# Kernel optimization log

Hardware: AMD Instinct MI355X
Metric: run time of the kernel (lower is better)

Reference implementation:

```python
import jax, jax.numpy as jnp
import numpy as np

MIN_STATES = 4
MAX_STATES = 64
B, S, D_IN, D_ST = 32, 2048, 1024, 512


def _linear_init(k, out_dim, in_dim):
    k1, k2 = jax.random.split(k)
    s = 1.0 / np.sqrt(in_dim)
    W = jax.random.uniform(k1, (out_dim, in_dim), minval=-s, maxval=s, dtype=jnp.float32)
    b = jax.random.uniform(k2, (out_dim,), minval=-s, maxval=s, dtype=jnp.float32)
    return W, b


def setup_inputs() -> dict:
    key = jax.random.key(0)
    ks = jax.random.split(key, 8)
    # complexity estimator MLP: D_IN -> D_ST -> D_ST//2 -> 1
    W1, b1 = _linear_init(ks[0], D_ST, D_IN)
    W2, b2 = _linear_init(ks[1], D_ST // 2, D_ST)
    W3, b3 = _linear_init(ks[2], 1, D_ST // 2)
    # importance scorer MLP: D_ST -> D_ST//2 -> 1
    Ws1, bs1 = _linear_init(ks[3], D_ST // 2, D_ST)
    Ws2, bs2 = _linear_init(ks[4], 1, D_ST // 2)
    state_bank = jax.random.normal(ks[5], (MAX_STATES, D_ST), dtype=jnp.float32) * 0.02
    temperature = jnp.ones((1,), dtype=jnp.float32)
    x = jax.random.normal(ks[6], (B, S, D_IN), dtype=jnp.float32)
    return dict(x=x, W1=W1, b1=b1, W2=W2, b2=b2, W3=W3, b3=b3,
                Ws1=Ws1, bs1=bs1, Ws2=Ws2, bs2=bs2,
                state_bank=state_bank, temperature=temperature)


def reference(x, W1, b1, W2, b2, W3, b3, Ws1, bs1, Ws2, bs2, state_bank, temperature):
    # --- complexity: mean-pool over seq, 3-layer MLP with sigmoid ---
    x_pooled = x.mean(axis=1)                                   # [B, D_IN]
    h = jax.nn.relu(x_pooled @ W1.T + b1)                       # [B, D_ST]
    h = jax.nn.relu(h @ W2.T + b2)                              # [B, D_ST//2]
    complexity = jax.nn.sigmoid(h @ W3.T + b3)[:, 0]            # [B]
    # --- importance over state bank: 2-layer MLP + tempered softmax ---
    hs = jax.nn.relu(state_bank @ Ws1.T + bs1)                  # [MAX_STATES, D_ST//2]
    imp_logits = (hs @ Ws2.T + bs2)[:, 0]                       # [MAX_STATES]
    temp = jnp.maximum(jnp.abs(temperature), 0.1)[0]
    importance = jax.nn.softmax(imp_logits / temp)              # [MAX_STATES]
    # --- per-sample number of active states ---
    num_states = jnp.clip(
        jnp.round(MIN_STATES + complexity * (MAX_STATES - MIN_STATES)).astype(jnp.int32),
        MIN_STATES, MAX_STATES)                                 # [B]
    # --- vectorized top-k mask: rank of each state in descending importance ---
    order = jnp.argsort(-importance)                            # [MAX_STATES]
    ranks = jnp.argsort(order)                                  # ranks[i] = position of state i
    state_mask = ranks[None, :] < num_states[:, None]           # [B, MAX_STATES] bool
    allocated_states = jnp.broadcast_to(state_bank[None], (x.shape[0],) + state_bank.shape)
    return allocated_states, state_mask
```

## Files before the change

kernel.cpp:

```cpp
#include <hip/hip_runtime.h>

#define BB 32
#define SS 2048
#define DIN 1024
#define DST 512
#define DH 256
#define NST 64
#define SC 32
#define CHUNKS (SS / SC)

__device__ __forceinline__ float dot4(float4 a, float4 b) {
    return a.x * b.x + a.y * b.y + a.z * b.z + a.w * b.w;
}

__global__ void k1_pool_bcast(const float* __restrict__ x, const float* __restrict__ bank,
                              float* __restrict__ partial, float* __restrict__ out) {
    int blk = blockIdx.x;
    int t = threadIdx.x;
    if (blk < 2048) {
        int b = blk >> 6;
        int c = blk & 63;
        const float4* xp = (const float4*)(x + ((size_t)b * SS + (size_t)c * SC) * DIN);
        float4 acc = make_float4(0.f, 0.f, 0.f, 0.f);
#pragma unroll
        for (int s = 0; s < SC; ++s) {
            float4 v = xp[s * (DIN / 4) + t];
            acc.x += v.x; acc.y += v.y; acc.z += v.z; acc.w += v.w;
        }
        ((float4*)(partial + (size_t)blk * DIN))[t] = acc;
    } else {
        int idx = (blk - 2048) * 256 + t;
        ((float4*)out)[idx] = ((const float4*)bank)[idx & 8191];
    }
}

__global__ void k2_pool2(const float* __restrict__ partial, float* __restrict__ pooled) {
    int b = blockIdx.x;
    int t = threadIdx.x;
    const float4* src = (const float4*)(partial + (size_t)b * CHUNKS * DIN);
    float4 acc = make_float4(0.f, 0.f, 0.f, 0.f);
#pragma unroll 8
    for (int c = 0; c < CHUNKS; ++c) {
        float4 v = src[c * (DIN / 4) + t];
        acc.x += v.x; acc.y += v.y; acc.z += v.z; acc.w += v.w;
    }
    const float invS = 1.0f / (float)SS;
    acc.x *= invS; acc.y *= invS; acc.z *= invS; acc.w *= invS;
    ((float4*)(pooled + (size_t)b * DIN))[t] = acc;
}

__global__ void k3_layer1(const float* __restrict__ pooled,
                          const float* __restrict__ W1, const float* __restrict__ b1,
                          const float* __restrict__ Ws1, const float* __restrict__ bs1,
                          const float* __restrict__ bank,
                          float* __restrict__ h1, float* __restrict__ hs) {
    int g = blockIdx.x;
    int t = threadIdx.x;
    if (g < 64) {
        int b = t & 31;
        int j = g * 8 + (t >> 5);
        const float4* w = (const float4*)(W1 + (size_t)j * DIN);
        const float4* p = (const float4*)(pooled + (size_t)b * DIN);
        float a0 = 0.f, a1 = 0.f;
#pragma unroll 8
        for (int k = 0; k < DIN / 4; k += 2) {
            a0 += dot4(w[k], p[k]);
            a1 += dot4(w[k + 1], p[k + 1]);
        }
        h1[(size_t)b * DST + j] = fmaxf(a0 + a1 + b1[j], 0.f);
    } else {
        int g2 = g - 64;
        int i = t & 63;
        int j = g2 * 4 + (t >> 6);
        const float4* w = (const float4*)(Ws1 + (size_t)j * DST);
        const float4* s = (const float4*)(bank + (size_t)i * DST);
        float a0 = 0.f, a1 = 0.f;
#pragma unroll 8
        for (int k = 0; k < DST / 4; k += 2) {
            a0 += dot4(w[k], s[k]);
            a1 += dot4(w[k + 1], s[k + 1]);
        }
        hs[(size_t)i * DH + j] = fmaxf(a0 + a1 + bs1[j], 0.f);
    }
}

__global__ void k4_layer2(const float* __restrict__ h1,
                          const float* __restrict__ W2, const float* __restrict__ b2,
                          const float* __restrict__ hs,
                          const float* __restrict__ Ws2, const float* __restrict__ bs2,
                          const float* __restrict__ W3,
                          float* __restrict__ zpart, float* __restrict__ imp) {
    int g = blockIdx.x;
    int t = threadIdx.x;
    if (g < 32) {
        __shared__ float s_z[8][32];
        int b = t & 31;
        int jq = t >> 5;
        int j = g * 8 + jq;
        const float4* w = (const float4*)(W2 + (size_t)j * DST);
        const float4* p = (const float4*)(h1 + (size_t)b * DST);
        float a0 = 0.f, a1 = 0.f;
#pragma unroll 8
        for (int k = 0; k < DST / 4; k += 2) {
            a0 += dot4(w[k], p[k]);
            a1 += dot4(w[k + 1], p[k + 1]);
        }
        float h2v = fmaxf(a0 + a1 + b2[j], 0.f);
        s_z[jq][b] = h2v * W3[j];
        __syncthreads();
        if (t < 32) {
            float z = 0.f;
#pragma unroll
            for (int q = 0; q < 8; ++q) z += s_z[q][t];
            zpart[g * 32 + t] = z;
        }
    } else {
        __shared__ float s_p[4][NST];
        int i = t & 63;
        int part = t >> 6;
        const float4* hv = (const float4*)(hs + (size_t)i * DH + part * 64);
        const float4* wv = (const float4*)(Ws2 + part * 64);
        float a = 0.f;
#pragma unroll
        for (int m = 0; m < 16; ++m) a += dot4(hv[m], wv[m]);
        s_p[part][i] = a;
        __syncthreads();
        if (t < NST) imp[t] = s_p[0][t] + s_p[1][t] + s_p[2][t] + s_p[3][t] + bs2[0];
    }
}

__global__ void k5_final(const float* __restrict__ zpart, const float* __restrict__ b3,
                         const float* __restrict__ imp, float* __restrict__ mask_out) {
    __shared__ float s_imp[NST];
    __shared__ int s_rank[NST];
    __shared__ int s_num[BB];
    int t = threadIdx.x;
    if (t < NST) s_imp[t] = imp[t];
    if (t < BB) {
        float z = 0.f;
        for (int g = 0; g < 32; ++g) z += zpart[g * 32 + t];
        z += b3[0];
        float cx = 1.0f / (1.0f + expf(-z));
        int ns = (int)rintf(4.0f + cx * 60.0f);
        s_num[t] = min(max(ns, 4), 64);
    }
    __syncthreads();
    if (t < NST) {
        float mine = s_imp[t];
        int r = 0;
        for (int j = 0; j < NST; ++j) {
            float o = s_imp[j];
            if (o > mine || (o == mine && j < t)) ++r;
        }
        s_rank[t] = r;
    }
    __syncthreads();
    for (int idx = t; idx < BB * NST; idx += 256)
        mask_out[idx] = (s_rank[idx & 63] < s_num[idx >> 6]) ? 1.0f : 0.0f;
}

extern "C" void kernel_launch(void* const* d_in, const int* in_sizes, int n_in,
                              void* d_out, int out_size, void* d_ws, size_t ws_size,
                              hipStream_t stream) {
    const float* x    = (const float*)d_in[0];
    const float* W1   = (const float*)d_in[1];
    const float* b1   = (const float*)d_in[2];
    const float* W2   = (const float*)d_in[3];
    const float* b2   = (const float*)d_in[4];
    const float* W3   = (const float*)d_in[5];
    const float* b3   = (const float*)d_in[6];
    const float* Ws1  = (const float*)d_in[7];
    const float* bs1  = (const float*)d_in[8];
    const float* Ws2  = (const float*)d_in[9];
    const float* bs2  = (const float*)d_in[10];
    const float* bank = (const float*)d_in[11];

    float* out = (float*)d_out;
    float* mask_out = out + (size_t)BB * NST * DST;

    float* ws = (float*)d_ws;
    float* partial = ws;
    float* pooled  = partial + (size_t)BB * CHUNKS * DIN;
    float* h1  = pooled + BB * DIN;
    float* hs  = h1 + BB * DST;
    float* zpart = hs + NST * DH;
    float* imp = zpart + 1024;

    k1_pool_bcast<<<3072, 256, 0, stream>>>(x, bank, partial, out);
    k2_pool2<<<BB, 256, 0, stream>>>(partial, pooled);
    k3_layer1<<<128, 256, 0, stream>>>(pooled, W1, b1, Ws1, bs1, bank, h1, hs);
    k4_layer2<<<33, 256, 0, stream>>>(h1, W2, b2, hs, Ws2, bs2, W3, zpart, imp);
    k5_final<<<1, 256, 0, stream>>>(zpart, b3, imp, mask_out);
}
```

Measured before the change: 121.9 us.

## Fuse pipeline into three kernels with wave-reduced matvecs

Collapses five launches into three. The importance MLP is folded into the pooling/broadcast kernel as 64 extra blocks. The second pooling stage is fused with layer 1, and layer 2 is fused with the final mask computation. Matvecs now use one wave per output row with shuffle reductions instead of one thread per row, which removes intermediate buffers and launch gaps. In exchange, the pool-2 reduction is recomputed in each of the four blocks per batch row, and layer-2 per-block work is serialized over 64 iterations.

```diff
diff --git a/kernel.cpp b/kernel.cpp
--- a/kernel.cpp
+++ b/kernel.cpp
@@ -13,30 +13,68 @@
     return a.x * b.x + a.y * b.y + a.z * b.z + a.w * b.w;
 }
 
-__global__ void k1_pool_bcast(const float* __restrict__ x, const float* __restrict__ bank,
-                              float* __restrict__ partial, float* __restrict__ out) {
+__device__ __forceinline__ float wave_reduce(float d) {
+    d += __shfl_xor(d, 1);
+    d += __shfl_xor(d, 2);
+    d += __shfl_xor(d, 4);
+    d += __shfl_xor(d, 8);
+    d += __shfl_xor(d, 16);
+    d += __shfl_xor(d, 32);
+    return d;
+}
+
+__global__ void k1_pool_imp_bcast(const float* __restrict__ x,
+                                  const float* __restrict__ bank,
+                                  const float* __restrict__ Ws1, const float* __restrict__ bs1,
+                                  const float* __restrict__ Ws2, const float* __restrict__ bs2,
+                                  float* __restrict__ partial, float* __restrict__ imp,
+                                  float* __restrict__ out) {
     int blk = blockIdx.x;
     int t = threadIdx.x;
-    if (blk < 2048) {
-        int b = blk >> 6;
-        int c = blk & 63;
+    if (blk >= 64 && blk < 64 + 2048) {
+        int task = blk - 64;
+        int b = task >> 6;
+        int c = task & 63;
         const float4* xp = (const float4*)(x + ((size_t)b * SS + (size_t)c * SC) * DIN);
         float4 acc = make_float4(0.f, 0.f, 0.f, 0.f);
-#pragma unroll
+#pragma unroll 8
         for (int s = 0; s < SC; ++s) {
             float4 v = xp[s * (DIN / 4) + t];
             acc.x += v.x; acc.y += v.y; acc.z += v.z; acc.w += v.w;
         }
-        ((float4*)(partial + (size_t)blk * DIN))[t] = acc;
+        ((float4*)(partial + (size_t)task * DIN))[t] = acc;
+    } else if (blk < 64) {
+        int i = blk;
+        int w = t >> 6, lane = t & 63;
+        __shared__ float s_zp[4];
+        const float4* brow = (const float4*)(bank + (size_t)i * DST);
+        float4 p0 = brow[lane * 2];
+        float4 p1 = brow[lane * 2 + 1];
+        float zacc = 0.f;
+        for (int jt = 0; jt < 64; ++jt) {
+            int j = jt * 4 + w;
+            const float4* wrow = (const float4*)(Ws1 + (size_t)j * DST);
+            float d = dot4(wrow[lane * 2], p0) + dot4(wrow[lane * 2 + 1], p1);
+            d = wave_reduce(d);
+            if (lane == 0) zacc += fmaxf(d + bs1[j], 0.f) * Ws2[j];
+        }
+        if (lane == 0) s_zp[w] = zacc;
+        __syncthreads();
+        if (t == 0) imp[i] = s_zp[0] + s_zp[1] + s_zp[2] + s_zp[3] + bs2[0];
     } else {
-        int idx = (blk - 2048) * 256 + t;
+        int idx = (blk - 2112) * 256 + t;
         ((float4*)out)[idx] = ((const float4*)bank)[idx & 8191];
     }
 }
 
-__global__ void k2_pool2(const float* __restrict__ partial, float* __restrict__ pooled) {
-    int b = blockIdx.x;
+__global__ void k2_h1(const float* __restrict__ partial,
+                      const float* __restrict__ W1, const float* __restrict__ b1,
+                      float* __restrict__ h1) {
+    int blk = blockIdx.x;
     int t = threadIdx.x;
+    int b = blk >> 2, jc = blk & 3;
+    __shared__ float4 s_pool[256];
+
     const float4* src = (const float4*)(partial + (size_t)b * CHUNKS * DIN);
     float4 acc = make_float4(0.f, 0.f, 0.f, 0.f);
 #pragma unroll 8
@@ -46,103 +84,55 @@
     }
     const float invS = 1.0f / (float)SS;
     acc.x *= invS; acc.y *= invS; acc.z *= invS; acc.w *= invS;
-    ((float4*)(pooled + (size_t)b * DIN))[t] = acc;
-}
+    s_pool[t] = acc;
+    __syncthreads();
 
-__global__ void k3_layer1(const float* __restrict__ pooled,
-                          const float* __restrict__ W1, const float* __restrict__ b1,
-                          const float* __restrict__ Ws1, const float* __restrict__ bs1,
-                          const float* __restrict__ bank,
-                          float* __restrict__ h1, float* __restrict__ hs) {
-    int g = blockIdx.x;
-    int t = threadIdx.x;
-    if (g < 64) {
-        int b = t & 31;
-        int j = g * 8 + (t >> 5);
-        const float4* w = (const float4*)(W1 + (size_t)j * DIN);
-        const float4* p = (const float4*)(pooled + (size_t)b * DIN);
-        float a0 = 0.f, a1 = 0.f;
-#pragma unroll 8
-        for (int k = 0; k < DIN / 4; k += 2) {
-            a0 += dot4(w[k], p[k]);
-            a1 += dot4(w[k + 1], p[k + 1]);
-        }
-        h1[(size_t)b * DST + j] = fmaxf(a0 + a1 + b1[j], 0.f);
-    } else {
-        int g2 = g - 64;
-        int i = t & 63;
-        int j = g2 * 4 + (t >> 6);
-        const float4* w = (const float4*)(Ws1 + (size_t)j * DST);
-        const float4* s = (const float4*)(bank + (size_t)i * DST);
-        float a0 = 0.f, a1 = 0.f;
-#pragma unroll 8
-        for (int k = 0; k < DST / 4; k += 2) {
-            a0 += dot4(w[k], s[k]);
-            a1 += dot4(w[k + 1], s[k + 1]);
-        }
-        hs[(size_t)i * DH + j] = fmaxf(a0 + a1 + bs1[j], 0.f);
+    int w = t >> 6, lane = t & 63;
+    float4 p[4];
+#pragma unroll
+    for (int m = 0; m < 4; ++m) p[m] = s_pool[lane * 4 + m];
+    for (int jt = 0; jt < 32; ++jt) {
+        int j = jc * 128 + jt * 4 + w;
+        const float4* wrow = (const float4*)(W1 + (size_t)j * DIN);
+        float d = 0.f;
+#pragma unroll
+        for (int m = 0; m < 4; ++m) d += dot4(wrow[lane * 4 + m], p[m]);
+        d = wave_reduce(d);
+        if (lane == 0) h1[(size_t)b * DST + j] = fmaxf(d + b1[j], 0.f);
     }
 }
 
-__global__ void k4_layer2(const float* __restrict__ h1,
-                          const float* __restrict__ W2, const float* __restrict__ b2,
-                          const float* __restrict__ hs,
-                          const float* __restrict__ Ws2, const float* __restrict__ bs2,
-                          const float* __restrict__ W3,
-                          float* __restrict__ zpart, float* __restrict__ imp) {
-    int g = blockIdx.x;
+__global__ void k3_final(const float* __restrict__ h1,
+                         const float* __restrict__ W2, const float* __restrict__ b2,
+                         const float* __restrict__ W3, const float* __restrict__ b3,
+                         const float* __restrict__ imp,
+                         float* __restrict__ mask_out) {
+    int b = blockIdx.x;
     int t = threadIdx.x;
-    if (g < 32) {
-        __shared__ float s_z[8][32];
-        int b = t & 31;
-        int jq = t >> 5;
-        int j = g * 8 + jq;
-        const float4* w = (const float4*)(W2 + (size_t)j * DST);
-        const float4* p = (const float4*)(h1 + (size_t)b * DST);
-        float a0 = 0.f, a1 = 0.f;
-#pragma unroll 8
-        for (int k = 0; k < DST / 4; k += 2) {
-            a0 += dot4(w[k], p[k]);
-            a1 += dot4(w[k + 1], p[k + 1]);
-        }
-        float h2v = fmaxf(a0 + a1 + b2[j], 0.f);
-        s_z[jq][b] = h2v * W3[j];
-        __syncthreads();
-        if (t < 32) {
-            float z = 0.f;
-#pragma unroll
-            for (int q = 0; q < 8; ++q) z += s_z[q][t];
-            zpart[g * 32 + t] = z;
-        }
-    } else {
-        __shared__ float s_p[4][NST];
-        int i = t & 63;
-        int part = t >> 6;
-        const float4* hv = (const float4*)(hs + (size_t)i * DH + part * 64);
-        const float4* wv = (const float4*)(Ws2 + part * 64);
-        float a = 0.f;
-#pragma unroll
-        for (int m = 0; m < 16; ++m) a += dot4(hv[m], wv[m]);
-        s_p[part][i] = a;
-        __syncthreads();
-        if (t < NST) imp[t] = s_p[0][t] + s_p[1][t] + s_p[2][t] + s_p[3][t] + bs2[0];
+    int w = t >> 6, lane = t & 63;
+    __shared__ float s_zp[4];
+    __shared__ float s_imp[NST];
+    __shared__ int s_ns;
+
+    const float4* hrow = (const float4*)(h1 + (size_t)b * DST);
+    float4 h0 = hrow[lane * 2];
+    float4 h1r = hrow[lane * 2 + 1];
+    float zacc = 0.f;
+    for (int jt = 0; jt < 64; ++jt) {
+        int j = jt * 4 + w;
+        const float4* wrow = (const float4*)(W2 + (size_t)j * DST);
+        float d = dot4(wrow[lane * 2], h0) + dot4(wrow[lane * 2 + 1], h1r);
+        d = wave_reduce(d);
+        if (lane == 0) zacc += fmaxf(d + b2[j], 0.f) * W3[j];
     }
-}
-
-__global__ void k5_final(const float* __restrict__ zpart, const float* __restrict__ b3,
-                         const float* __restrict__ imp, float* __restrict__ mask_out) {
-    __shared__ float s_imp[NST];
-    __shared__ int s_rank[NST];
-    __shared__ int s_num[BB];
-    int t = threadIdx.x;
+    if (lane == 0) s_zp[w] = zacc;
     if (t < NST) s_imp[t] = imp[t];
-    if (t < BB) {
-        float z = 0.f;
-        for (int g = 0; g < 32; ++g) z += zpart[g * 32 + t];
-        z += b3[0];
+    __syncthreads();
+    if (t == 0) {
+        float z = s_zp[0] + s_zp[1] + s_zp[2] + s_zp[3] + b3[0];
         float cx = 1.0f / (1.0f + expf(-z));
         int ns = (int)rintf(4.0f + cx * 60.0f);
-        s_num[t] = min(max(ns, 4), 64);
+        s_ns = min(max(ns, 4), 64);
     }
     __syncthreads();
     if (t < NST) {
@@ -152,11 +142,8 @@
             float o = s_imp[j];
             if (o > mine || (o == mine && j < t)) ++r;
         }
-        s_rank[t] = r;
+        mask_out[b * NST + t] = (r < s_ns) ? 1.0f : 0.0f;
     }
-    __syncthreads();
-    for (int idx = t; idx < BB * NST; idx += 256)
-        mask_out[idx] = (s_rank[idx & 63] < s_num[idx >> 6]) ? 1.0f : 0.0f;
 }
 
 extern "C" void kernel_launch(void* const* d_in, const int* in_sizes, int n_in,
@@ -180,15 +167,11 @@
 
     float* ws = (float*)d_ws;
     float* partial = ws;
-    float* pooled  = partial + (size_t)BB * CHUNKS * DIN;
-    float* h1  = pooled + BB * DIN;
-    float* hs  = h1 + BB * DST;
-    float* zpart = hs + NST * DH;
-    float* imp = zpart + 1024;
+    float* h1  = partial + (size_t)BB * CHUNKS * DIN;
+    float* imp = h1 + (size_t)BB * DST;
 
-    k1_pool_bcast<<<3072, 256, 0, stream>>>(x, bank, partial, out);
-    k2_pool2<<<BB, 256, 0, stream>>>(partial, pooled);
-    k3_layer1<<<128, 256, 0, stream>>>(pooled, W1, b1, Ws1, bs1, bank, h1, hs);
-    k4_layer2<<<33, 256, 0, stream>>>(h1, W2, b2, hs, Ws2, bs2, W3, zpart, imp);
-    k5_final<<<1, 256, 0, stream>>>(zpart, b3, imp, mask_out);
+    k1_pool_imp_bcast<<<3136, 256, 0, stream>>>(x, bank, Ws1, bs1, Ws2, bs2,
+                                                partial, imp, out);
+    k2_h1<<<128, 256, 0, stream>>>(partial, W1, b1, h1);
+    k3_final<<<32, 256, 0, stream>>>(h1, W2, b2, W3, b3, imp, mask_out);
 }
```

New measurement: 140.6 us. +15.4%, slower.
